# Kernel tuning notes

Measured on AMD Instinct MI355X. Metric: run time of the kernel, lower is better.

Reference implementation:

```python
import jax, jax.numpy as jnp
import numpy as np

D = 128          # fine voxel grid resolution
N0 = 250000
D_IN, D_BASE, D_OUT = 16, 8, 8
EPS = 1e-5
# (cin, cout) for conv0..conv6, conv7, conv9, conv11
_CH = [(16, 8), (8, 16), (16, 16), (16, 32), (32, 32), (32, 64), (64, 64), (64, 32), (32, 16), (16, 8)]

def _offsets():
    r = np.arange(-1, 2)
    return np.stack(np.meshgrid(r, r, r, indexing='ij'), -1).reshape(-1, 3)  # [27,3]

def _lookup_fn(coords, d):
    keys = (coords[:, 0].astype(np.int64) * d + coords[:, 1]) * d + coords[:, 2]
    order = np.argsort(keys)
    skeys = keys[order]
    def lookup(q):
        valid = ((q >= 0) & (q < d)).all(-1)
        k = (q[:, 0].astype(np.int64) * d + q[:, 1]) * d + q[:, 2]
        pos = np.clip(np.searchsorted(skeys, k), 0, len(skeys) - 1)
        return np.where(valid & (skeys[pos] == k), order[pos], -1).astype(np.int32)
    return lookup

def _nbr_same(coords, d):
    # stride-1 sparse conv: outputs at input coords, neighbors at coord+k
    lk = _lookup_fn(coords, d)
    return np.stack([lk(coords + o) for o in _offsets()], 1)  # [N,27]

def _nbr_down(c_out, c_in, d_in):
    # stride-2 conv: output p gathers inputs at 2p+k
    lk = _lookup_fn(c_in, d_in)
    return np.stack([lk(c_out * 2 + o) for o in _offsets()], 1)

def _nbr_up(c_out, c_in, d_in):
    # transposed stride-2 conv: output q gathers input p=(q-k)/2 where divisible
    lk = _lookup_fn(c_in, d_in)
    cols = []
    for o in _offsets():
        q = c_out - o
        div = (q % 2 == 0).all(-1)
        cols.append(np.where(div, lk(q // 2), -1).astype(np.int32))
    return np.stack(cols, 1)

def setup_inputs():
    rng = np.random.default_rng(0)
    flat = rng.choice(D ** 3, size=N0, replace=False)
    c0 = np.stack([flat // (D * D), (flat // D) % D, flat % D], 1).astype(np.int32)
    c1 = np.unique(c0 // 2, axis=0)
    c2 = np.unique(c1 // 2, axis=0)
    c3 = np.unique(c2 // 2, axis=0)
    inp = {
        'feats': jax.random.normal(jax.random.key(0), (N0, D_IN), jnp.float32),
        'nbr0': jnp.asarray(_nbr_same(c0, D)),
        'nbr_d01': jnp.asarray(_nbr_down(c1, c0, D)),
        'nbr1': jnp.asarray(_nbr_same(c1, D // 2)),
        'nbr_d12': jnp.asarray(_nbr_down(c2, c1, D // 2)),
        'nbr2': jnp.asarray(_nbr_same(c2, D // 4)),
        'nbr_d23': jnp.asarray(_nbr_down(c3, c2, D // 4)),
        'nbr3': jnp.asarray(_nbr_same(c3, D // 8)),
        'nbr_u32': jnp.asarray(_nbr_up(c2, c3, D // 8)),
        'nbr_u21': jnp.asarray(_nbr_up(c1, c2, D // 4)),
        'nbr_u10': jnp.asarray(_nbr_up(c0, c1, D // 2)),
    }
    key = jax.random.key(1)
    for i, (ci, co) in enumerate(_CH):
        key, kw = jax.random.split(key)
        inp['w%d' % i] = jax.random.normal(kw, (27, ci, co), jnp.float32) / np.sqrt(27.0 * ci)
        inp['g%d' % i] = jnp.ones((co,), jnp.float32)
        inp['b%d' % i] = jnp.zeros((co,), jnp.float32)
    inp['lin_w'] = jax.random.normal(jax.random.key(2), (D_OUT, D_BASE), jnp.float32) / np.sqrt(D_BASE)
    return inp

def _sconv_bn_relu(f, nbr, w, g, b):
    # f: [Nin,Cin], nbr: [Nout,27] (-1 = no neighbor), w: [27,Cin,Cout]
    gth = jnp.where((nbr >= 0)[..., None], f[jnp.maximum(nbr, 0)], 0.0)  # [Nout,27,Cin]
    y = jnp.einsum('nkc,kco->no', gth, w)
    mu = y.mean(0)                       # training-mode BatchNorm over active voxels
    var = y.var(0)
    return jax.nn.relu((y - mu) * jax.lax.rsqrt(var + EPS) * g + b)

def reference(feats, nbr0, nbr_d01, nbr1, nbr_d12, nbr2, nbr_d23, nbr3, nbr_u32, nbr_u21, nbr_u10,
              w0, g0, b0, w1, g1, b1, w2, g2, b2, w3, g3, b3, w4, g4, b4,
              w5, g5, b5, w6, g6, b6, w7, g7, b7, w8, g8, b8, w9, g9, b9, lin_w):
    c0f = _sconv_bn_relu(feats, nbr0, w0, g0, b0)
    c2f = _sconv_bn_relu(_sconv_bn_relu(c0f, nbr_d01, w1, g1, b1), nbr1, w2, g2, b2)
    c4f = _sconv_bn_relu(_sconv_bn_relu(c2f, nbr_d12, w3, g3, b3), nbr2, w4, g4, b4)
    x = _sconv_bn_relu(_sconv_bn_relu(c4f, nbr_d23, w5, g5, b5), nbr3, w6, g6, b6)
    x = c4f + _sconv_bn_relu(x, nbr_u32, w7, g7, b7)
    x = c2f + _sconv_bn_relu(x, nbr_u21, w8, g8, b8)
    x = c0f + _sconv_bn_relu(x, nbr_u10, w9, g9, b9)
    return x @ lin_w.T, x
```

## Files before the change

kernel.cpp:

```cpp
#include <hip/hip_runtime.h>

#define EPSV 1e-5f

typedef __attribute__((ext_vector_type(8))) short short8;
typedef __attribute__((ext_vector_type(4))) float float4v;

static inline int cdiv(int a, int b) { return (a + b - 1) / b; }
static inline int imin(int a, int b) { return a < b ? a : b; }

__device__ inline unsigned short f2bf(float x) {
  unsigned u = __float_as_uint(x);
  return (unsigned short)((u + 0x7FFFu + ((u >> 16) & 1u)) >> 16);
}
__device__ inline float bf2f(unsigned short u) {
  return __uint_as_float(((unsigned)u) << 16);
}

#define NBUCKET 64

struct PrepArgs {
  const float* w[10];
  unsigned short* wt[10];
  int ci[10];
  int co[10];
  int wcum[11];
  const float* feats;
  unsigned short* featsb;
  int nfeat4;
  float* stats;
};

__global__ __launch_bounds__(256) void prep_kernel(PrepArgs p, long total) {
  const int nstat4 = 10 * NBUCKET * 128 / 4;
  for (long tid0 = (long)blockIdx.x * 256 + threadIdx.x; tid0 < total;
       tid0 += (long)gridDim.x * 256) {
    long tid = tid0;
    if (tid < nstat4) {
      ((float4*)p.stats)[tid] = make_float4(0.f, 0.f, 0.f, 0.f);
      continue;
    }
    tid -= nstat4;
    if (tid < p.nfeat4) {
      float4 v = ((const float4*)p.feats)[tid];
      ushort4 r;
      r.x = f2bf(v.x); r.y = f2bf(v.y); r.z = f2bf(v.z); r.w = f2bf(v.w);
      ((ushort4*)p.featsb)[tid] = r;
      continue;
    }
    tid -= p.nfeat4;
    if (tid >= p.wcum[10]) continue;
    int i = 0;
    while (tid >= p.wcum[i + 1]) ++i;
    int e = (int)(tid - p.wcum[i]);
    int ci = p.ci[i], co = p.co[i];
    int k = e / (ci * co);
    int r = e - k * (ci * co);
    int o = r / ci;
    int c = r - o * ci;
    p.wt[i][((long)k * co + o) * ci + c] = f2bf(p.w[i][((long)k * ci + c) * co + o]);
  }
}

template<int CI, int CO, int MINW>
__global__ __launch_bounds__(256, MINW) void conv_mfma(
    const unsigned short* __restrict__ f, const int* __restrict__ nbr,
    const unsigned short* __restrict__ wt, unsigned short* __restrict__ y,
    float* __restrict__ stats, int nout, int ntiles) {
  constexpr int NCHUNK = (CI == 8) ? 7 : (CI == 16) ? 14 : (CI == 32) ? 27 : 54;
  constexpr int CIP = (CI == 64) ? 64 : (CI == 32) ? 40 : 24;

  __shared__ int nbrT[64 * 27];
  __shared__ unsigned short Bs[27 * 16 * CIP];

  const int tid = threadIdx.x;
  const int lane = tid & 63;
  const int wid = tid >> 6;
  const int m = lane & 15;
  const int quad = lane >> 4;
  const int cbase = blockIdx.y * 16;
  const int co = cbase + m;
  const bool cok = co < CO;

  auto tapof = [&](int c) -> int {
    if constexpr (CI == 8) return c * 4 + quad;
    else if constexpr (CI == 16) return c * 2 + (quad >> 1);
    else if constexpr (CI == 32) return c;
    else return c >> 1;
  };
  auto cioof = [&](int c) -> int {
    if constexpr (CI == 8) return 0;
    else if constexpr (CI == 16) return (quad & 1) * 8;
    else if constexpr (CI == 32) return quad * 8;
    else return ((c & 1) << 5) + quad * 8;
  };
  auto baddr = [&](int tap, int mm, int cio) -> int {
    if constexpr (CI == 64) {
      int byt = (tap * 16 + mm) * 128 + cio * 2;
      byt ^= (mm & 7) << 4;
      return byt >> 1;
    } else {
      return (tap * 16 + mm) * CIP + cio;
    }
  };

  {
    constexpr int NC8 = CI / 8;
    for (int t = tid; t < 27 * 16 * NC8; t += 256) {
      int tap = t / (16 * NC8);
      int r = t - tap * (16 * NC8);
      int mo = r / NC8;
      int c8 = (r - mo * NC8) * 8;
      short8 v;
#pragma unroll
      for (int q = 0; q < 8; ++q) v[q] = 0;
      int c = cbase + mo;
      if (c < CO) v = *(const short8*)(wt + ((long)tap * CO + c) * CI + c8);
      *(short8*)&Bs[baddr(tap, mo, c8)] = v;
    }
  }

  float sum = 0.f, sq = 0.f;

  for (int tile = blockIdx.x; tile < ntiles; tile += gridDim.x) {
    const int rowb0 = tile * 64;
    {
      const int base = rowb0 * 27;
      const int lim = nout * 27;
      for (int j = tid; j < 432; j += 256) {
        int e = j * 4;
        int g = base + e;
        int4 v;
        if (g + 4 <= lim) {
          v = *(const int4*)(nbr + g);
        } else {
          v.x = (g + 0 < lim) ? nbr[g + 0] : -1;
          v.y = (g + 1 < lim) ? nbr[g + 1] : -1;
          v.z = (g + 2 < lim) ? nbr[g + 2] : -1;
          v.w = (g + 3 < lim) ? nbr[g + 3] : -1;
        }
        *(int4*)&nbrT[e] = v;
      }
    }
    __syncthreads();

    const int rowb = rowb0 + wid * 16;
    const int lrow = (wid * 16 + m) * 27;

    if constexpr (CI <= 16) {
      int idxs[NCHUNK];
#pragma unroll
      for (int c = 0; c < NCHUNK; ++c) {
        int tap = tapof(c);
        idxs[c] = (tap < 27) ? nbrT[lrow + tap] : -1;
      }
      short8 A[NCHUNK];
#pragma unroll
      for (int c = 0; c < NCHUNK; ++c) {
        short8 a;
#pragma unroll
        for (int q = 0; q < 8; ++q) a[q] = 0;
        if (idxs[c] >= 0) a = *(const short8*)(f + (long)idxs[c] * CI + cioof(c));
        A[c] = a;
      }
      float4v acc = {0.f, 0.f, 0.f, 0.f};
#pragma unroll
      for (int c = 0; c < NCHUNK; ++c) {
        int tap = tapof(c);
        int tapc = tap < 27 ? tap : 26;
        short8 bf = *(const short8*)&Bs[baddr(tapc, m, cioof(c))];
        acc = __builtin_amdgcn_mfma_f32_16x16x32_bf16(A[c], bf, acc, 0, 0, 0);
      }
#pragma unroll
      for (int r = 0; r < 4; ++r) {
        float v = acc[r];
        int orow = rowb + quad * 4 + r;
        if (cok && orow < nout) y[(long)orow * CO + co] = f2bf(v);
        sum += v;
        sq = fmaf(v, v, sq);
      }
    } else {
      constexpr int G = 9;
      constexpr int NG = NCHUNK / G;
      short8 A[2][G];
      auto load_group = [&](int g, int bi) {
#pragma unroll
        for (int j = 0; j < G; ++j) {
          const int c = g * G + j;
          const int tap = tapof(c);
          int idx = nbrT[lrow + tap];
          short8 a;
#pragma unroll
          for (int q = 0; q < 8; ++q) a[q] = 0;
          if (idx >= 0) a = *(const short8*)(f + (long)idx * CI + cioof(c));
          A[bi][j] = a;
        }
      };
      float4v acc = {0.f, 0.f, 0.f, 0.f};
      load_group(0, 0);
#pragma unroll
      for (int g = 0; g < NG; ++g) {
        const int cur = g & 1;
        if (g + 1 < NG) load_group(g + 1, cur ^ 1);
#pragma unroll
        for (int j = 0; j < G; ++j) {
          const int c = g * G + j;
          short8 bf = *(const short8*)&Bs[baddr(tapof(c), m, cioof(c))];
          acc = __builtin_amdgcn_mfma_f32_16x16x32_bf16(A[cur][j], bf, acc, 0, 0, 0);
        }
      }
#pragma unroll
      for (int r = 0; r < 4; ++r) {
        float v = acc[r];
        int orow = rowb + quad * 4 + r;
        if (cok && orow < nout) y[(long)orow * CO + co] = f2bf(v);
        sum += v;
        sq = fmaf(v, v, sq);
      }
    }
    __syncthreads();
  }

  sum += __shfl_xor(sum, 16); sq += __shfl_xor(sq, 16);
  sum += __shfl_xor(sum, 32); sq += __shfl_xor(sq, 32);
  if (quad == 0 && cok) {
    float* st = stats + ((((unsigned)blockIdx.x * 4 + wid) & (NBUCKET - 1)) << 7);
    atomicAdd(&st[co], sum);
    atomicAdd(&st[64 + co], sq);
  }
}

template<int CO>
__global__ __launch_bounds__(256) void bn_relu_bf16(
    const unsigned short* __restrict__ y, const float* __restrict__ stats,
    const float* __restrict__ g, const float* __restrict__ b,
    const unsigned short* __restrict__ skip, unsigned short* __restrict__ out,
    int nout, float inv_n) {
  __shared__ float sA[CO], sC[CO];
  if ((int)threadIdx.x < CO) {
    int o = threadIdx.x;
    float su = 0.f, sq = 0.f;
#pragma unroll 8
    for (int bk = 0; bk < NBUCKET; ++bk) {
      su += stats[bk * 128 + o];
      sq += stats[bk * 128 + 64 + o];
    }
    float mu = su * inv_n;
    float var = sq * inv_n - mu * mu;
    float a = g[o] * rsqrtf(var + EPSV);
    sA[o] = a;
    sC[o] = fmaf(-mu, a, b[o]);
  }
  __syncthreads();
  long total4 = (long)nout * CO / 4;
  for (long i4 = (long)blockIdx.x * 256 + threadIdx.x; i4 < total4;
       i4 += (long)gridDim.x * 256) {
    int o = (int)((i4 * 4) % CO);
    ushort4 v = ((const ushort4*)y)[i4];
    float vv[4] = {bf2f(v.x), bf2f(v.y), bf2f(v.z), bf2f(v.w)};
    unsigned short rr[4];
#pragma unroll
    for (int j = 0; j < 4; ++j) {
      float x = fmaxf(fmaf(vv[j], sA[o + j], sC[o + j]), 0.f);
      if (skip) x += bf2f(skip[i4 * 4 + j]);
      rr[j] = f2bf(x);
    }
    ushort4 r;
    r.x = rr[0]; r.y = rr[1]; r.z = rr[2]; r.w = rr[3];
    ((ushort4*)out)[i4] = r;
  }
}

__global__ __launch_bounds__(256) void tail_kernel(
    const unsigned short* __restrict__ c0f, const float* __restrict__ st9,
    const float* __restrict__ g9, const float* __restrict__ b9, float inv_n,
    const float* __restrict__ lin_w, const unsigned short* __restrict__ y9,
    float* __restrict__ out0, float* __restrict__ x0, int n0) {
  __shared__ float swl[64];
  __shared__ float sbn[16];
  if (threadIdx.x < 64) swl[threadIdx.x] = lin_w[threadIdx.x];
  if (threadIdx.x < 8) {
    int o = threadIdx.x;
    float su = 0.f, sq = 0.f;
#pragma unroll 8
    for (int bk = 0; bk < NBUCKET; ++bk) {
      su += st9[bk * 128 + o];
      sq += st9[bk * 128 + 64 + o];
    }
    float mu = su * inv_n;
    float var = sq * inv_n - mu * mu;
    float a = g9[o] * rsqrtf(var + EPSV);
    sbn[o] = a;
    sbn[8 + o] = fmaf(-mu, a, b9[o]);
  }
  __syncthreads();
  for (int n = blockIdx.x * 256 + threadIdx.x; n < n0; n += gridDim.x * 256) {
    const ushort4* pr = (const ushort4*)(y9 + (long)n * 8);
    ushort4 r0 = pr[0], r1 = pr[1];
    unsigned short rw[8] = {r0.x, r0.y, r0.z, r0.w, r1.x, r1.y, r1.z, r1.w};
    const ushort4* pc = (const ushort4*)(c0f + (long)n * 8);
    ushort4 c0 = pc[0], c1 = pc[1];
    unsigned short cs[8] = {c0.x, c0.y, c0.z, c0.w, c1.x, c1.y, c1.z, c1.w};
    float xv[8];
#pragma unroll
    for (int c = 0; c < 8; ++c)
      xv[c] = bf2f(cs[c]) + fmaxf(fmaf(bf2f(rw[c]), sbn[c], sbn[8 + c]), 0.f);
    *(float4*)(x0 + (long)n * 8) = make_float4(xv[0], xv[1], xv[2], xv[3]);
    *(float4*)(x0 + (long)n * 8 + 4) = make_float4(xv[4], xv[5], xv[6], xv[7]);
    float ov[8];
#pragma unroll
    for (int j = 0; j < 8; ++j) {
      float s = 0.f;
#pragma unroll
      for (int c = 0; c < 8; ++c) s = fmaf(xv[c], swl[j * 8 + c], s);
      ov[j] = s;
    }
    *(float4*)(out0 + (long)n * 8) = make_float4(ov[0], ov[1], ov[2], ov[3]);
    *(float4*)(out0 + (long)n * 8 + 4) = make_float4(ov[4], ov[5], ov[6], ov[7]);
  }
}

extern "C" void kernel_launch(void* const* d_in, const int* in_sizes, int n_in,
                              void* d_out, int out_size, void* d_ws, size_t ws_size,
                              hipStream_t stream) {
  const float* feats   = (const float*)d_in[0];
  const int* nbr0      = (const int*)d_in[1];
  const int* nbr_d01   = (const int*)d_in[2];
  const int* nbr1      = (const int*)d_in[3];
  const int* nbr_d12   = (const int*)d_in[4];
  const int* nbr2      = (const int*)d_in[5];
  const int* nbr_d23   = (const int*)d_in[6];
  const int* nbr3      = (const int*)d_in[7];
  const int* nbr_u32   = (const int*)d_in[8];
  const int* nbr_u21   = (const int*)d_in[9];
  const int* nbr_u10   = (const int*)d_in[10];
  const float* w[10];
  const float* g[10];
  const float* b[10];
  for (int i = 0; i < 10; ++i) {
    w[i] = (const float*)d_in[11 + 3 * i];
    g[i] = (const float*)d_in[12 + 3 * i];
    b[i] = (const float*)d_in[13 + 3 * i];
  }
  const float* lin_w = (const float*)d_in[41];

  const int N0 = in_sizes[0] / 16;
  const int N1 = in_sizes[2] / 27;
  const int N2 = in_sizes[4] / 27;
  const int N3 = in_sizes[6] / 27;
  const float i0 = 1.f / N0, i1 = 1.f / N1, i2 = 1.f / N2, i3 = 1.f / N3;

  static const int CIv[10] = {16, 8, 16, 16, 32, 32, 64, 64, 32, 16};
  static const int COv[10] = {8, 16, 16, 32, 32, 64, 64, 32, 16, 8};

  float* stats = (float*)d_ws;
  unsigned short* u = (unsigned short*)(stats + 10 * NBUCKET * 128);

  unsigned short* yraw = u; u += (size_t)N1 * 32;

  unsigned short* wt[10];
  int wcum[11];
  wcum[0] = 0;
  for (int i = 0; i < 10; ++i) {
    wt[i] = u;
    int sz = 27 * CIv[i] * COv[i];
    u += sz;
    wcum[i + 1] = wcum[i] + sz;
  }
  unsigned short* featsb = u; u += (size_t)N0 * 16;
  unsigned short* c0f = u;    u += (size_t)N0 * 8;
  unsigned short* t1  = u;    u += (size_t)N1 * 16;
  unsigned short* c2f = u;    u += (size_t)N1 * 16;
  unsigned short* t2  = u;    u += (size_t)N2 * 32;
  unsigned short* c4f = u;    u += (size_t)N2 * 32;
  unsigned short* t3  = u;    u += (size_t)N3 * 64;
  unsigned short* t4  = u;    u += (size_t)N3 * 64;
  unsigned short* t5  = t2;
  unsigned short* t6  = t1;
  float* out0 = (float*)d_out;
  float* x0   = (float*)d_out + (size_t)N0 * 8;

  float* s[10];
  for (int i = 0; i < 10; ++i) s[i] = stats + i * NBUCKET * 128;

  PrepArgs pa;
  for (int i = 0; i < 10; ++i) {
    pa.w[i] = w[i]; pa.wt[i] = wt[i];
    pa.ci[i] = CIv[i]; pa.co[i] = COv[i];
    pa.wcum[i] = wcum[i];
  }
  pa.wcum[10] = wcum[10];
  pa.feats = feats; pa.featsb = featsb;
  pa.nfeat4 = N0 * 16 / 4;
  pa.stats = stats;
  long prep_total = (10 * NBUCKET * 128 / 4) + pa.nfeat4 + wcum[10];
  prep_kernel<<<imin((int)((prep_total + 255) / 256), 2048), 256, 0, stream>>>(pa, prep_total);

  auto bgrid = [](long nout, int co) {
    return imin((int)((nout * co / 4 + 255) / 256), 1024);
  };
  auto cgrid = [](int ntiles) { return imin(ntiles, 2048); };

  int tb0 = cdiv(N0, 64), tb1 = cdiv(N1, 64), tb2 = cdiv(N2, 64), tb3 = cdiv(N3, 64);

  conv_mfma<16, 8, 4><<<dim3(cgrid(tb0), 1), 256, 0, stream>>>(featsb, nbr0, wt[0], yraw, s[0], N0, tb0);
  bn_relu_bf16<8><<<bgrid(N0, 8), 256, 0, stream>>>(yraw, s[0], g[0], b[0], nullptr, c0f, N0, i0);

  conv_mfma<8, 16, 4><<<dim3(cgrid(tb1), 1), 256, 0, stream>>>(c0f, nbr_d01, wt[1], yraw, s[1], N1, tb1);
  bn_relu_bf16<16><<<bgrid(N1, 16), 256, 0, stream>>>(yraw, s[1], g[1], b[1], nullptr, t1, N1, i1);

  conv_mfma<16, 16, 4><<<dim3(cgrid(tb1), 1), 256, 0, stream>>>(t1, nbr1, wt[2], yraw, s[2], N1, tb1);
  bn_relu_bf16<16><<<bgrid(N1, 16), 256, 0, stream>>>(yraw, s[2], g[2], b[2], nullptr, c2f, N1, i1);

  conv_mfma<16, 32, 4><<<dim3(cgrid(tb2), 2), 256, 0, stream>>>(c2f, nbr_d12, wt[3], yraw, s[3], N2, tb2);
  bn_relu_bf16<32><<<bgrid(N2, 32), 256, 0, stream>>>(yraw, s[3], g[3], b[3], nullptr, t2, N2, i2);

  conv_mfma<32, 32, 3><<<dim3(cgrid(tb2), 2), 256, 0, stream>>>(t2, nbr2, wt[4], yraw, s[4], N2, tb2);
  bn_relu_bf16<32><<<bgrid(N2, 32), 256, 0, stream>>>(yraw, s[4], g[4], b[4], nullptr, c4f, N2, i2);

  conv_mfma<32, 64, 3><<<dim3(cgrid(tb3), 4), 256, 0, stream>>>(c4f, nbr_d23, wt[5], yraw, s[5], N3, tb3);
  bn_relu_bf16<64><<<bgrid(N3, 64), 256, 0, stream>>>(yraw, s[5], g[5], b[5], nullptr, t3, N3, i3);

  conv_mfma<64, 64, 2><<<dim3(cgrid(tb3), 4), 256, 0, stream>>>(t3, nbr3, wt[6], yraw, s[6], N3, tb3);
  bn_relu_bf16<64><<<bgrid(N3, 64), 256, 0, stream>>>(yraw, s[6], g[6], b[6], nullptr, t4, N3, i3);

  conv_mfma<64, 32, 2><<<dim3(cgrid(tb2), 2), 256, 0, stream>>>(t4, nbr_u32, wt[7], yraw, s[7], N2, tb2);
  bn_relu_bf16<32><<<bgrid(N2, 32), 256, 0, stream>>>(yraw, s[7], g[7], b[7], c4f, t5, N2, i2);

  conv_mfma<32, 16, 3><<<dim3(cgrid(tb1), 1), 256, 0, stream>>>(t5, nbr_u21, wt[8], yraw, s[8], N1, tb1);
  bn_relu_bf16<16><<<bgrid(N1, 16), 256, 0, stream>>>(yraw, s[8], g[8], b[8], c2f, t6, N1, i1);

  conv_mfma<16, 8, 4><<<dim3(cgrid(tb0), 1), 256, 0, stream>>>(t6, nbr_u10, wt[9], yraw, s[9], N0, tb0);

  tail_kernel<<<imin(cdiv(N0, 256), 1024), 256, 0, stream>>>(
      c0f, s[9], g[9], b[9], i0, lin_w, yraw, out0, x0, N0);
}
```

Baseline: 427.9 us.

## Fuse BatchNorm+ReLU of previous layer into sparse conv gather

New measurement: 474.8 us. 1.11x slower.

```diff
diff --git a/kernel.cpp b/kernel.cpp
--- a/kernel.cpp
+++ b/kernel.cpp
@@ -1,6 +1,7 @@
 #include <hip/hip_runtime.h>
 
 #define EPSV 1e-5f
+#define NBUCKET 64
 
 typedef __attribute__((ext_vector_type(8))) short short8;
 typedef __attribute__((ext_vector_type(4))) float float4v;
@@ -15,8 +16,6 @@
 __device__ inline float bf2f(unsigned short u) {
   return __uint_as_float(((unsigned)u) << 16);
 }
-
-#define NBUCKET 64
 
 struct PrepArgs {
   const float* w[10];
@@ -61,16 +60,21 @@
   }
 }
 
-template<int CI, int CO, int MINW>
+template<int CI, int CO, bool FUSED, int MINW>
 __global__ __launch_bounds__(256, MINW) void conv_mfma(
     const unsigned short* __restrict__ f, const int* __restrict__ nbr,
     const unsigned short* __restrict__ wt, unsigned short* __restrict__ y,
-    float* __restrict__ stats, int nout, int ntiles) {
+    float* __restrict__ stats,
+    const float* __restrict__ fstats, const float* __restrict__ fg,
+    const float* __restrict__ fb, float finv_n,
+    int nout, int ntiles) {
   constexpr int NCHUNK = (CI == 8) ? 7 : (CI == 16) ? 14 : (CI == 32) ? 27 : 54;
   constexpr int CIP = (CI == 64) ? 64 : (CI == 32) ? 40 : 24;
+  constexpr int NFR = (CI == 64) ? 16 : 8;
 
   __shared__ int nbrT[64 * 27];
   __shared__ unsigned short Bs[27 * 16 * CIP];
+  __shared__ float fsh[FUSED ? 2 * CI : 4];
 
   const int tid = threadIdx.x;
   const int lane = tid & 63;
@@ -103,6 +107,22 @@
     }
   };
 
+  if constexpr (FUSED) {
+    for (int o = tid; o < CI; o += 256) {
+      float su = 0.f, sq = 0.f;
+#pragma unroll 8
+      for (int bk = 0; bk < NBUCKET; ++bk) {
+        su += fstats[bk * 128 + o];
+        sq += fstats[bk * 128 + 64 + o];
+      }
+      float mu = su * finv_n;
+      float var = sq * finv_n - mu * mu;
+      float a = fg[o] * rsqrtf(var + EPSV);
+      fsh[o] = a;
+      fsh[CI + o] = fmaf(-mu, a, fb[o]);
+    }
+  }
+
   {
     constexpr int NC8 = CI / 8;
     for (int t = tid; t < 27 * 16 * NC8; t += 256) {
@@ -118,17 +138,51 @@
       *(short8*)&Bs[baddr(tap, mo, c8)] = v;
     }
   }
+  __syncthreads();
+
+  float fAr[NFR], fCr[NFR];
+  if constexpr (FUSED) {
+    if constexpr (CI == 64) {
+#pragma unroll
+      for (int h = 0; h < 2; ++h)
+#pragma unroll
+        for (int q = 0; q < 8; ++q) {
+          fAr[h * 8 + q] = fsh[h * 32 + quad * 8 + q];
+          fCr[h * 8 + q] = fsh[CI + h * 32 + quad * 8 + q];
+        }
+    } else {
+      const int cio0 = (CI == 8) ? 0 : (CI == 16) ? (quad & 1) * 8 : quad * 8;
+#pragma unroll
+      for (int q = 0; q < 8; ++q) {
+        fAr[q] = fsh[cio0 + q];
+        fCr[q] = fsh[CI + cio0 + q];
+      }
+    }
+  } else {
+    (void)fAr; (void)fCr;
+  }
+
+  auto fuse8 = [&](short8 a, int fb8) -> short8 {
+    if constexpr (FUSED) {
+#pragma unroll
+      for (int q = 0; q < 8; ++q) {
+        float v = bf2f((unsigned short)a[q]);
+        v = fmaxf(fmaf(v, fAr[fb8 + q], fCr[fb8 + q]), 0.f);
+        a[q] = (short)f2bf(v);
+      }
+    }
+    return a;
+  };
 
   float sum = 0.f, sq = 0.f;
 
   for (int tile = blockIdx.x; tile < ntiles; tile += gridDim.x) {
     const int rowb0 = tile * 64;
     {
-      const int base = rowb0 * 27;
-      const int lim = nout * 27;
+      const long base = (long)rowb0 * 27;
+      const long lim = (long)nout * 27;
       for (int j = tid; j < 432; j += 256) {
-        int e = j * 4;
-        int g = base + e;
+        long g = base + j * 4;
         int4 v;
         if (g + 4 <= lim) {
           v = *(const int4*)(nbr + g);
@@ -138,13 +192,14 @@
           v.z = (g + 2 < lim) ? nbr[g + 2] : -1;
           v.w = (g + 3 < lim) ? nbr[g + 3] : -1;
         }
-        *(int4*)&nbrT[e] = v;
+        *(int4*)&nbrT[j * 4] = v;
       }
     }
     __syncthreads();
 
     const int rowb = rowb0 + wid * 16;
     const int lrow = (wid * 16 + m) * 27;
+    float4v acc = {0.f, 0.f, 0.f, 0.f};
 
     if constexpr (CI <= 16) {
       int idxs[NCHUNK];
@@ -159,10 +214,9 @@
         short8 a;
 #pragma unroll
         for (int q = 0; q < 8; ++q) a[q] = 0;
-        if (idxs[c] >= 0) a = *(const short8*)(f + (long)idxs[c] * CI + cioof(c));
+        if (idxs[c] >= 0) a = fuse8(*(const short8*)(f + (long)idxs[c] * CI + cioof(c)), 0);
         A[c] = a;
       }
-      float4v acc = {0.f, 0.f, 0.f, 0.f};
 #pragma unroll
       for (int c = 0; c < NCHUNK; ++c) {
         int tap = tapof(c);
@@ -170,14 +224,6 @@
         short8 bf = *(const short8*)&Bs[baddr(tapc, m, cioof(c))];
         acc = __builtin_amdgcn_mfma_f32_16x16x32_bf16(A[c], bf, acc, 0, 0, 0);
       }
-#pragma unroll
-      for (int r = 0; r < 4; ++r) {
-        float v = acc[r];
-        int orow = rowb + quad * 4 + r;
-        if (cok && orow < nout) y[(long)orow * CO + co] = f2bf(v);
-        sum += v;
-        sq = fmaf(v, v, sq);
-      }
     } else {
       constexpr int G = 9;
       constexpr int NG = NCHUNK / G;
@@ -191,11 +237,12 @@
           short8 a;
 #pragma unroll
           for (int q = 0; q < 8; ++q) a[q] = 0;
-          if (idx >= 0) a = *(const short8*)(f + (long)idx * CI + cioof(c));
+          if (idx >= 0)
+            a = fuse8(*(const short8*)(f + (long)idx * CI + cioof(c)),
+                      (CI == 64) ? ((c & 1) * 8) : 0);
           A[bi][j] = a;
         }
       };
-      float4v acc = {0.f, 0.f, 0.f, 0.f};
       load_group(0, 0);
 #pragma unroll
       for (int g = 0; g < NG; ++g) {
@@ -208,14 +255,15 @@
           acc = __builtin_amdgcn_mfma_f32_16x16x32_bf16(A[cur][j], bf, acc, 0, 0, 0);
         }
       }
-#pragma unroll
-      for (int r = 0; r < 4; ++r) {
-        float v = acc[r];
-        int orow = rowb + quad * 4 + r;
-        if (cok && orow < nout) y[(long)orow * CO + co] = f2bf(v);
-        sum += v;
-        sq = fmaf(v, v, sq);
-      }
+    }
+
+#pragma unroll
+    for (int r = 0; r < 4; ++r) {
+      float v = acc[r];
+      int orow = rowb + quad * 4 + r;
+      if (cok && orow < nout) y[(long)orow * CO + co] = f2bf(v);
+      sum += v;
+      sq = fmaf(v, v, sq);
     }
     __syncthreads();
   }
@@ -230,25 +278,32 @@
 }
 
 template<int CO>
-__global__ __launch_bounds__(256) void bn_relu_bf16(
-    const unsigned short* __restrict__ y, const float* __restrict__ stats,
-    const float* __restrict__ g, const float* __restrict__ b,
-    const unsigned short* __restrict__ skip, unsigned short* __restrict__ out,
-    int nout, float inv_n) {
-  __shared__ float sA[CO], sC[CO];
-  if ((int)threadIdx.x < CO) {
-    int o = threadIdx.x;
-    float su = 0.f, sq = 0.f;
+__global__ __launch_bounds__(256) void bn_dual(
+    const unsigned short* __restrict__ y, const float* __restrict__ st,
+    const float* __restrict__ g, const float* __restrict__ b, float inv_n,
+    const unsigned short* __restrict__ ys, const float* __restrict__ sts,
+    const float* __restrict__ gs, const float* __restrict__ bs, float inv_ns,
+    unsigned short* __restrict__ out, int nout) {
+  __shared__ float sA[CO], sC[CO], sAs[CO], sCs[CO];
+  for (int o = threadIdx.x; o < CO; o += 256) {
+    float su = 0.f, sq = 0.f, sus = 0.f, sqs = 0.f;
 #pragma unroll 8
     for (int bk = 0; bk < NBUCKET; ++bk) {
-      su += stats[bk * 128 + o];
-      sq += stats[bk * 128 + 64 + o];
+      su += st[bk * 128 + o];
+      sq += st[bk * 128 + 64 + o];
+      sus += sts[bk * 128 + o];
+      sqs += sts[bk * 128 + 64 + o];
     }
     float mu = su * inv_n;
     float var = sq * inv_n - mu * mu;
     float a = g[o] * rsqrtf(var + EPSV);
     sA[o] = a;
     sC[o] = fmaf(-mu, a, b[o]);
+    float mus = sus * inv_ns;
+    float vars = sqs * inv_ns - mus * mus;
+    float as = gs[o] * rsqrtf(vars + EPSV);
+    sAs[o] = as;
+    sCs[o] = fmaf(-mus, as, bs[o]);
   }
   __syncthreads();
   long total4 = (long)nout * CO / 4;
@@ -256,13 +311,15 @@
        i4 += (long)gridDim.x * 256) {
     int o = (int)((i4 * 4) % CO);
     ushort4 v = ((const ushort4*)y)[i4];
+    ushort4 w = ((const ushort4*)ys)[i4];
     float vv[4] = {bf2f(v.x), bf2f(v.y), bf2f(v.z), bf2f(v.w)};
+    float ww[4] = {bf2f(w.x), bf2f(w.y), bf2f(w.z), bf2f(w.w)};
     unsigned short rr[4];
 #pragma unroll
     for (int j = 0; j < 4; ++j) {
       float x = fmaxf(fmaf(vv[j], sA[o + j], sC[o + j]), 0.f);
-      if (skip) x += bf2f(skip[i4 * 4 + j]);
-      rr[j] = f2bf(x);
+      float sk = bf2f(f2bf(fmaxf(fmaf(ww[j], sAs[o + j], sCs[o + j]), 0.f)));
+      rr[j] = f2bf(x + sk);
     }
     ushort4 r;
     r.x = rr[0]; r.y = rr[1]; r.z = rr[2]; r.w = rr[3];
@@ -271,39 +328,50 @@
 }
 
 __global__ __launch_bounds__(256) void tail_kernel(
-    const unsigned short* __restrict__ c0f, const float* __restrict__ st9,
-    const float* __restrict__ g9, const float* __restrict__ b9, float inv_n,
+    const unsigned short* __restrict__ y0, const float* __restrict__ st0,
+    const float* __restrict__ g0, const float* __restrict__ b0,
+    const float* __restrict__ st9, const float* __restrict__ g9,
+    const float* __restrict__ b9, float inv_n,
     const float* __restrict__ lin_w, const unsigned short* __restrict__ y9,
     float* __restrict__ out0, float* __restrict__ x0, int n0) {
   __shared__ float swl[64];
-  __shared__ float sbn[16];
+  __shared__ float sbn9[16], sbn0[16];
   if (threadIdx.x < 64) swl[threadIdx.x] = lin_w[threadIdx.x];
   if (threadIdx.x < 8) {
     int o = threadIdx.x;
-    float su = 0.f, sq = 0.f;
+    float su = 0.f, sq = 0.f, su0 = 0.f, sq0 = 0.f;
 #pragma unroll 8
     for (int bk = 0; bk < NBUCKET; ++bk) {
       su += st9[bk * 128 + o];
       sq += st9[bk * 128 + 64 + o];
+      su0 += st0[bk * 128 + o];
+      sq0 += st0[bk * 128 + 64 + o];
     }
     float mu = su * inv_n;
     float var = sq * inv_n - mu * mu;
     float a = g9[o] * rsqrtf(var + EPSV);
-    sbn[o] = a;
-    sbn[8 + o] = fmaf(-mu, a, b9[o]);
+    sbn9[o] = a;
+    sbn9[8 + o] = fmaf(-mu, a, b9[o]);
+    float mu0 = su0 * inv_n;
+    float var0 = sq0 * inv_n - mu0 * mu0;
+    float a0 = g0[o] * rsqrtf(var0 + EPSV);
+    sbn0[o] = a0;
+    sbn0[8 + o] = fmaf(-mu0, a0, b0[o]);
   }
   __syncthreads();
-  for (int n = blockIdx.x * 256 + threadIdx.x; n < n0; n += gridDim.x * 256) {
+  for (int n = blockIdx.x * 256 + (int)threadIdx.x; n < n0; n += gridDim.x * 256) {
     const ushort4* pr = (const ushort4*)(y9 + (long)n * 8);
     ushort4 r0 = pr[0], r1 = pr[1];
     unsigned short rw[8] = {r0.x, r0.y, r0.z, r0.w, r1.x, r1.y, r1.z, r1.w};
-    const ushort4* pc = (const ushort4*)(c0f + (long)n * 8);
+    const ushort4* pc = (const ushort4*)(y0 + (long)n * 8);
     ushort4 c0 = pc[0], c1 = pc[1];
     unsigned short cs[8] = {c0.x, c0.y, c0.z, c0.w, c1.x, c1.y, c1.z, c1.w};
     float xv[8];
 #pragma unroll
-    for (int c = 0; c < 8; ++c)
-      xv[c] = bf2f(cs[c]) + fmaxf(fmaf(bf2f(rw[c]), sbn[c], sbn[8 + c]), 0.f);
+    for (int c = 0; c < 8; ++c) {
+      float c0f = bf2f(f2bf(fmaxf(fmaf(bf2f(cs[c]), sbn0[c], sbn0[8 + c]), 0.f)));
+      xv[c] = c0f + fmaxf(fmaf(bf2f(rw[c]), sbn9[c], sbn9[8 + c]), 0.f);
+    }
     *(float4*)(x0 + (long)n * 8) = make_float4(xv[0], xv[1], xv[2], xv[3]);
     *(float4*)(x0 + (long)n * 8 + 4) = make_float4(xv[4], xv[5], xv[6], xv[7]);
     float ov[8];
@@ -322,17 +390,17 @@
 extern "C" void kernel_launch(void* const* d_in, const int* in_sizes, int n_in,
                               void* d_out, int out_size, void* d_ws, size_t ws_size,
                               hipStream_t stream) {
-  const float* feats   = (const float*)d_in[0];
-  const int* nbr0      = (const int*)d_in[1];
-  const int* nbr_d01   = (const int*)d_in[2];
-  const int* nbr1      = (const int*)d_in[3];
-  const int* nbr_d12   = (const int*)d_in[4];
-  const int* nbr2      = (const int*)d_in[5];
-  const int* nbr_d23   = (const int*)d_in[6];
-  const int* nbr3      = (const int*)d_in[7];
-  const int* nbr_u32   = (const int*)d_in[8];
-  const int* nbr_u21   = (const int*)d_in[9];
-  const int* nbr_u10   = (const int*)d_in[10];
+  const float* feats = (const float*)d_in[0];
+  const int* nbr0    = (const int*)d_in[1];
+  const int* nbr_d01 = (const int*)d_in[2];
+  const int* nbr1    = (const int*)d_in[3];
+  const int* nbr_d12 = (const int*)d_in[4];
+  const int* nbr2    = (const int*)d_in[5];
+  const int* nbr_d23 = (const int*)d_in[6];
+  const int* nbr3    = (const int*)d_in[7];
+  const int* nbr_u32 = (const int*)d_in[8];
+  const int* nbr_u21 = (const int*)d_in[9];
+  const int* nbr_u10 = (const int*)d_in[10];
   const float* w[10];
   const float* g[10];
   const float* b[10];
@@ -354,8 +422,6 @@
 
   float* stats = (float*)d_ws;
   unsigned short* u = (unsigned short*)(stats + 10 * NBUCKET * 128);
-
-  unsigned short* yraw = u; u += (size_t)N1 * 32;
 
   unsigned short* wt[10];
   int wcum[11];
@@ -367,17 +433,20 @@
     wcum[i + 1] = wcum[i] + sz;
   }
   unsigned short* featsb = u; u += (size_t)N0 * 16;
-  unsigned short* c0f = u;    u += (size_t)N0 * 8;
-  unsigned short* t1  = u;    u += (size_t)N1 * 16;
-  unsigned short* c2f = u;    u += (size_t)N1 * 16;
-  unsigned short* t2  = u;    u += (size_t)N2 * 32;
-  unsigned short* c4f = u;    u += (size_t)N2 * 32;
-  unsigned short* t3  = u;    u += (size_t)N3 * 64;
-  unsigned short* t4  = u;    u += (size_t)N3 * 64;
-  unsigned short* t5  = t2;
-  unsigned short* t6  = t1;
+  unsigned short* y0 = u; u += (size_t)N0 * 8;
+  unsigned short* y1 = u; u += (size_t)N1 * 16;
+  unsigned short* y2 = u; u += (size_t)N1 * 16;
+  unsigned short* y3 = u; u += (size_t)N2 * 32;
+  unsigned short* y4 = u; u += (size_t)N2 * 32;
+  unsigned short* y5 = u; u += (size_t)N3 * 64;
+  unsigned short* y6 = u; u += (size_t)N3 * 64;
+  unsigned short* y7 = u; u += (size_t)N2 * 32;
+  unsigned short* y8 = u; u += (size_t)N1 * 16;
+  unsigned short* y9 = u; u += (size_t)N0 * 8;
+  unsigned short* t5 = u; u += (size_t)N2 * 32;
+  unsigned short* t6 = u; u += (size_t)N1 * 16;
   float* out0 = (float*)d_out;
-  float* x0   = (float*)d_out + (size_t)N0 * 8;
+  float* x0 = (float*)d_out + (size_t)N0 * 8;
 
   float* s[10];
   for (int i = 0; i < 10; ++i) s[i] = stats + i * NBUCKET * 128;
@@ -399,38 +468,32 @@
     return imin((int)((nout * co / 4 + 255) / 256), 1024);
   };
   auto cgrid = [](int ntiles) { return imin(ntiles, 2048); };
-
   int tb0 = cdiv(N0, 64), tb1 = cdiv(N1, 64), tb2 = cdiv(N2, 64), tb3 = cdiv(N3, 64);
 
-  conv_mfma<16, 8, 4><<<dim3(cgrid(tb0), 1), 256, 0, stream>>>(featsb, nbr0, wt[0], yraw, s[0], N0, tb0);
-  bn_relu_bf16<8><<<bgrid(N0, 8), 256, 0, stream>>>(yraw, s[0], g[0], b[0], nullptr, c0f, N0, i0);
-
-  conv_mfma<8, 16, 4><<<dim3(cgrid(tb1), 1), 256, 0, stream>>>(c0f, nbr_d01, wt[1], yraw, s[1], N1, tb1);
-  bn_relu_bf16<16><<<bgrid(N1, 16), 256, 0, stream>>>(yraw, s[1], g[1], b[1], nullptr, t1, N1, i1);
-
-  conv_mfma<16, 16, 4><<<dim3(cgrid(tb1), 1), 256, 0, stream>>>(t1, nbr1, wt[2], yraw, s[2], N1, tb1);
-  bn_relu_bf16<16><<<bgrid(N1, 16), 256, 0, stream>>>(yraw, s[2], g[2], b[2], nullptr, c2f, N1, i1);
-
-  conv_mfma<16, 32, 4><<<dim3(cgrid(tb2), 2), 256, 0, stream>>>(c2f, nbr_d12, wt[3], yraw, s[3], N2, tb2);
-  bn_relu_bf16<32><<<bgrid(N2, 32), 256, 0, stream>>>(yraw, s[3], g[3], b[3], nullptr, t2, N2, i2);
-
-  conv_mfma<32, 32, 3><<<dim3(cgrid(tb2), 2), 256, 0, stream>>>(t2, nbr2, wt[4], yraw, s[4], N2, tb2);
-  bn_relu_bf16<32><<<bgrid(N2, 32), 256, 0, stream>>>(yraw, s[4], g[4], b[4], nullptr, c4f, N2, i2);
-
-  conv_mfma<32, 64, 3><<<dim3(cgrid(tb3), 4), 256, 0, stream>>>(c4f, nbr_d23, wt[5], yraw, s[5], N3, tb3);
-  bn_relu_bf16<64><<<bgrid(N3, 64), 256, 0, stream>>>(yraw, s[5], g[5], b[5], nullptr, t3, N3, i3);
-
-  conv_mfma<64, 64, 2><<<dim3(cgrid(tb3), 4), 256, 0, stream>>>(t3, nbr3, wt[6], yraw, s[6], N3, tb3);
-  bn_relu_bf16<64><<<bgrid(N3, 64), 256, 0, stream>>>(yraw, s[6], g[6], b[6], nullptr, t4, N3, i3);
-
-  conv_mfma<64, 32, 2><<<dim3(cgrid(tb2), 2), 256, 0, stream>>>(t4, nbr_u32, wt[7], yraw, s[7], N2, tb2);
-  bn_relu_bf16<32><<<bgrid(N2, 32), 256, 0, stream>>>(yraw, s[7], g[7], b[7], c4f, t5, N2, i2);
-
-  conv_mfma<32, 16, 3><<<dim3(cgrid(tb1), 1), 256, 0, stream>>>(t5, nbr_u21, wt[8], yraw, s[8], N1, tb1);
-  bn_relu_bf16<16><<<bgrid(N1, 16), 256, 0, stream>>>(yraw, s[8], g[8], b[8], c2f, t6, N1, i1);
-
-  conv_mfma<16, 8, 4><<<dim3(cgrid(tb0), 1), 256, 0, stream>>>(t6, nbr_u10, wt[9], yraw, s[9], N0, tb0);
-
+  conv_mfma<16, 8, false, 4><<<dim3(cgrid(tb0), 1), 256, 0, stream>>>(
+      featsb, nbr0, wt[0], y0, s[0], nullptr, nullptr, nullptr, 0.f, N0, tb0);
+  conv_mfma<8, 16, true, 4><<<dim3(cgrid(tb1), 1), 256, 0, stream>>>(
+      y0, nbr_d01, wt[1], y1, s[1], s[0], g[0], b[0], i0, N1, tb1);
+  conv_mfma<16, 16, true, 4><<<dim3(cgrid(tb1), 1), 256, 0, stream>>>(
+      y1, nbr1, wt[2], y2, s[2], s[1], g[1], b[1], i1, N1, tb1);
+  conv_mfma<16, 32, true, 4><<<dim3(cgrid(tb2), 2), 256, 0, stream>>>(
+      y2, nbr_d12, wt[3], y3, s[3], s[2], g[2], b[2], i1, N2, tb2);
+  conv_mfma<32, 32, true, 3><<<dim3(cgrid(tb2), 2), 256, 0, stream>>>(
+      y3, nbr2, wt[4], y4, s[4], s[3], g[3], b[3], i2, N2, tb2);
+  conv_mfma<32, 64, true, 3><<<dim3(cgrid(tb3), 4), 256, 0, stream>>>(
+      y4, nbr_d23, wt[5], y5, s[5], s[4], g[4], b[4], i2, N3, tb3);
+  conv_mfma<64, 64, true, 2><<<dim3(cgrid(tb3), 4), 256, 0, stream>>>(
+      y5, nbr3, wt[6], y6, s[6], s[5], g[5], b[5], i3, N3, tb3);
+  conv_mfma<64, 32, true, 2><<<dim3(cgrid(tb2), 2), 256, 0, stream>>>(
+      y6, nbr_u32, wt[7], y7, s[7], s[6], g[6], b[6], i3, N2, tb2);
+  bn_dual<32><<<bgrid(N2, 32), 256, 0, stream>>>(
+      y7, s[7], g[7], b[7], i2, y4, s[4], g[4], b[4], i2, t5, N2);
+  conv_mfma<32, 16, false, 3><<<dim3(cgrid(tb1), 1), 256, 0, stream>>>(
+      t5, nbr_u21, wt[8], y8, s[8], nullptr, nullptr, nullptr, 0.f, N1, tb1);
+  bn_dual<16><<<bgrid(N1, 16), 256, 0, stream>>>(
+      y8, s[8], g[8], b[8], i1, y2, s[2], g[2], b[2], i1, t6, N1);
+  conv_mfma<16, 8, false, 4><<<dim3(cgrid(tb0), 1), 256, 0, stream>>>(
+      t6, nbr_u10, wt[9], y9, s[9], nullptr, nullptr, nullptr, 0.f, N0, tb0);
   tail_kernel<<<imin(cdiv(N0, 256), 1024), 256, 0, stream>>>(
-      c0f, s[9], g[9], b[9], i0, lin_w, yraw, out0, x0, N0);
-}
+      y0, s[0], g[0], b[0], s[9], g[9], b[9], i0, lin_w, y9, out0, x0, N0);
+}
```
